# Kernel optimization log

Hardware: AMD Instinct MI355X
Metric: run time of the kernel (lower is better)

Reference implementation:

```python
import jax, jax.numpy as jnp
import numpy as np

SHAPES = ((496, 432), (248, 216), (124, 108))
NS = (40000, 20000, 8000)
T = 32
B = 4
EPS = 1e-3


def _bn(x, g, b, m, v):
    return (x - m) * (g / jnp.sqrt(v + EPS)) + b


def _vfe_scale(voxels, num_pts, w1, p1, w2, p2):
    # voxels: (N, T, 4); num_pts: (N,)
    Tp = voxels.shape[1]
    n = num_pts.astype(voxels.dtype)[:, None, None]
    m3 = voxels[:, :, :3].sum(axis=1, keepdims=True) / n
    m2 = voxels[:, :, :2].sum(axis=1, keepdims=True) / n
    feat = jnp.concatenate([voxels[:, :, :4], voxels[:, :, :3] - m3, voxels[:, :, :2] - m2], axis=-1)  # (N,T,9)
    mask = (jnp.arange(Tp)[None, :] < num_pts[:, None]).astype(voxels.dtype)[:, :, None]
    x = feat
    for w, (g, b_, rm, rv) in ((w1, p1), (w2, p2)):
        h = jax.nn.relu(_bn(jnp.einsum('ntc,cd->ntd', x, w), g, b_, rm, rv))  # (N,T,64)
        gmax = h.max(axis=1, keepdims=True)  # global max includes padded rows, as in torch source
        x = jnp.concatenate([h, jnp.broadcast_to(gmax, h.shape)], axis=-1) * mask  # (N,T,128)
    return x.max(axis=1)[:, :64]  # (N,64)


def _scatter_bev(vf, coords, h, w, batch_size):
    b = coords[:, 0]
    y = jnp.clip(coords[:, 2], 0, h - 1)
    x = jnp.clip(coords[:, 3], 0, w - 1)
    grid = jnp.zeros((batch_size, vf.shape[1], h, w), vf.dtype)
    return grid.at[b, :, y, x].set(vf)


def _fusion(x, w, g, b, m, v):
    y = jax.lax.conv_general_dilated(x, w, (1, 1), ((1, 1), (1, 1)),
                                     dimension_numbers=('NCHW', 'OIHW', 'NCHW'))
    y = _bn(y, g[None, :, None, None], b[None, :, None, None], m[None, :, None, None], v[None, :, None, None])
    return jax.nn.relu(y)


def setup_inputs() -> dict:
    key = jax.random.key(0)
    ks = jax.random.split(key, 32)
    inp = {}
    for s in range(3):
        h, w = SHAPES[s]
        inp[f'voxels_{s}'] = jax.random.normal(ks[s], (NS[s], T, 4), dtype=jnp.float32)
        inp[f'num_pts_{s}'] = jax.random.randint(ks[3 + s], (NS[s],), 1, T + 1, dtype=jnp.int32)
        b = jax.random.randint(ks[6 + s], (NS[s],), 0, B, dtype=jnp.int32)
        z = jnp.zeros((NS[s],), jnp.int32)
        y = jax.random.randint(ks[9 + s], (NS[s],), 0, h, dtype=jnp.int32)
        x = jax.random.randint(ks[12 + s], (NS[s],), 0, w, dtype=jnp.int32)
        inp[f'coords_{s}'] = jnp.stack([b, z, y, x], axis=1)
    # VFE params (stacked across the 3 scales; identical shapes per scale)
    inp['w1'] = jax.random.normal(ks[15], (3, 9, 64), dtype=jnp.float32) * 0.1
    inp['g1'] = jnp.ones((3, 64), jnp.float32) + 0.1 * jax.random.normal(ks[16], (3, 64))
    inp['b1'] = 0.05 * jax.random.normal(ks[17], (3, 64))
    inp['rm1'] = 0.05 * jax.random.normal(ks[18], (3, 64))
    inp['rv1'] = 0.5 + jnp.abs(jax.random.normal(ks[19], (3, 64)))
    inp['w2'] = jax.random.normal(ks[20], (3, 128, 64), dtype=jnp.float32) * 0.05
    inp['g2'] = jnp.ones((3, 64), jnp.float32) + 0.1 * jax.random.normal(ks[21], (3, 64))
    inp['b2'] = 0.05 * jax.random.normal(ks[22], (3, 64))
    inp['rm2'] = 0.05 * jax.random.normal(ks[23], (3, 64))
    inp['rv2'] = 0.5 + jnp.abs(jax.random.normal(ks[24], (3, 64)))
    # Fusion convs (2): Conv2d(128,64,3) + BN
    inp['fw'] = jax.random.normal(ks[25], (2, 64, 128, 3, 3), dtype=jnp.float32) * 0.03
    inp['fg'] = jnp.ones((2, 64), jnp.float32) + 0.1 * jax.random.normal(ks[26], (2, 64))
    inp['fb'] = 0.05 * jax.random.normal(ks[27], (2, 64))
    inp['fm'] = 0.05 * jax.random.normal(ks[28], (2, 64))
    inp['fv'] = 0.5 + jnp.abs(jax.random.normal(ks[29], (2, 64)))
    inp['batch_size'] = B
    return inp


def reference(voxels_0, voxels_1, voxels_2,
              w1, g1, b1, rm1, rv1, w2, g2, b2, rm2, rv2,
              fw, fg, fb, fm, fv,
              num_pts_0, num_pts_1, num_pts_2,
              coords_0, coords_1, coords_2, batch_size):
    voxels = (voxels_0, voxels_1, voxels_2)
    num_pts = (num_pts_0, num_pts_1, num_pts_2)
    coords = (coords_0, coords_1, coords_2)
    sf = []
    for s in range(3):
        vf = _vfe_scale(voxels[s], num_pts[s],
                        w1[s], (g1[s], b1[s], rm1[s], rv1[s]),
                        w2[s], (g2[s], b2[s], rm2[s], rv2[s]))
        h, w = SHAPES[s]
        sf.append(_scatter_bev(vf, coords[s], h, w, batch_size))
    # bottom-up fusion: scale2 -> scale1 -> scale0
    up = jax.image.resize(sf[2], sf[1].shape[:2] + SHAPES[1], method='bilinear')
    fused_1 = _fusion(jnp.concatenate([sf[1], up], axis=1), fw[1], fg[1], fb[1], fm[1], fv[1])
    up = jax.image.resize(fused_1, fused_1.shape[:2] + SHAPES[0], method='bilinear')
    fused_0 = _fusion(jnp.concatenate([sf[0], up], axis=1), fw[0], fg[0], fb[0], fm[0], fv[0])
    return fused_0  # spatial_features_2d: (B, 64, 496, 432)
```

## Files before the change

### kernel.cpp

```cpp
#include <hip/hip_runtime.h>

typedef unsigned short u16;
typedef short bf16x8 __attribute__((ext_vector_type(8)));
typedef float f32x4 __attribute__((ext_vector_type(4)));

#define EPSV 1e-3f

__device__ __forceinline__ float bf2f(u16 u) {
  union { unsigned int i; float f; } x; x.i = ((unsigned int)u) << 16; return x.f;
}
__device__ __forceinline__ u16 f2bf(float f) {
  union { float f; unsigned int i; } x; x.f = f;
  unsigned int r = x.i + 0x7fffu + ((x.i >> 16) & 1u);
  return (u16)(r >> 16);
}

#define WAVE_FENCE() do { __builtin_amdgcn_s_waitcnt(0); __builtin_amdgcn_wave_barrier(); } while (0)

__global__ void twt_kernel(const float* __restrict__ fw, u16* __restrict__ fwT) {
  int i = blockIdx.x * blockDim.x + threadIdx.x;
  if (i >= 2 * 9 * 64 * 128) return;
  int ci = i & 127;
  int r = i >> 7;
  int co = r & 63; r >>= 6;
  int kyx = r % 9;
  int set = r / 9;
  fwT[i] = f2bf(fw[(((set * 64 + co) * 128 + ci) * 9) + kyx]);
}

__global__ __launch_bounds__(256, 2) void vfe_mfma_kernel(
    const float* __restrict__ vox, const int* __restrict__ npts,
    const float* __restrict__ w1, const float* __restrict__ g1, const float* __restrict__ b1,
    const float* __restrict__ rm1, const float* __restrict__ rv1,
    const float* __restrict__ w2, const float* __restrict__ g2, const float* __restrict__ b2,
    const float* __restrict__ rm2, const float* __restrict__ rv2,
    float* __restrict__ vf, int N)
{
  struct PerWave {
    u16 X[32 * 72];
    u16 F[32 * 40];
    u16 G[64];
  };
  __shared__ __align__(16) union {
    struct { u16 W1T[64 * 40]; u16 W2T[64 * 136]; } w;
    PerWave r[4];
  } lds;

  const int tid = threadIdx.x;
  const int lane = tid & 63;
  const int wv = tid >> 6;
  const int m16 = lane & 15;
  const int q = lane >> 4;

  for (int i = tid; i < 64 * 40; i += 256) {
    int c = i / 40, k = i % 40;
    lds.w.W1T[i] = f2bf(k < 9 ? w1[k * 64 + c] : 0.f);
  }
  for (int i = tid; i < 64 * 136; i += 256) {
    int c = i / 136, j = i % 136;
    lds.w.W2T[i] = f2bf(j < 128 ? w2[j * 64 + c] : 0.f);
  }
  __syncthreads();

  bf16x8 bW1[4], bLo[4][2], bHi[4][2];
  float sc1[4], sh1[4], sc2[4], sh2[4];
#pragma unroll
  for (int nf = 0; nf < 4; ++nf) {
    int c = nf * 16 + m16;
    bW1[nf] = *(const bf16x8*)&lds.w.W1T[c * 40 + q * 8];
#pragma unroll
    for (int ks = 0; ks < 2; ++ks) {
      bLo[nf][ks] = *(const bf16x8*)&lds.w.W2T[c * 136 + ks * 32 + q * 8];
      bHi[nf][ks] = *(const bf16x8*)&lds.w.W2T[c * 136 + 64 + ks * 32 + q * 8];
    }
    float s1 = g1[c] * rsqrtf(rv1[c] + EPSV);
    sc1[nf] = s1; sh1[nf] = b1[c] - rm1[c] * s1;
    float s2 = g2[c] * rsqrtf(rv2[c] + EPSV);
    sc2[nf] = s2; sh2[nf] = b2[c] - rm2[c] * s2;
  }
  __syncthreads();

  u16* X = lds.r[wv].X;
  u16* F = lds.r[wv].F;
  u16* G = lds.r[wv].G;
  for (int i = lane; i < 640; i += 64) ((unsigned int*)F)[i] = 0u;

  const int wgid = blockIdx.x * 4 + wv;
  const int wstride = gridDim.x * 4;

  for (int v = wgid; v < N; v += wstride) {
    const int n = npts[v];
    float px = 0.f, py = 0.f, pz = 0.f, pw = 0.f;
    if (lane < 32) {
      float4 u = *(const float4*)(vox + ((size_t)v * 32 + lane) * 4);
      px = u.x; py = u.y; pz = u.z; pw = u.w;
    }
    float sx = px, sy = py, sz = pz;
#pragma unroll
    for (int off = 32; off >= 1; off >>= 1) {
      sx += __shfl_xor(sx, off);
      sy += __shfl_xor(sy, off);
      sz += __shfl_xor(sz, off);
    }
    float nf_ = (float)n;
    float mx = sx / nf_, my = sy / nf_, mz = sz / nf_;
    if (lane < 32) {
      float dx = px - mx, dy = py - my, dz = pz - mz;
      bf16x8 r0, r1;
      r0[0] = (short)f2bf(px); r0[1] = (short)f2bf(py);
      r0[2] = (short)f2bf(pz); r0[3] = (short)f2bf(pw);
      r0[4] = (short)f2bf(dx); r0[5] = (short)f2bf(dy);
      r0[6] = (short)f2bf(dz); r0[7] = (short)f2bf(dx);
      r1 = (bf16x8){0, 0, 0, 0, 0, 0, 0, 0};
      r1[0] = (short)f2bf(dy);
      *(bf16x8*)&F[lane * 40 + 0] = r0;
      *(bf16x8*)&F[lane * 40 + 8] = r1;
    }
    WAVE_FENCE();

    bf16x8 a1[2];
    a1[0] = *(const bf16x8*)&F[m16 * 40 + q * 8];
    a1[1] = *(const bf16x8*)&F[(16 + m16) * 40 + q * 8];
    f32x4 acc1[2][4];
#pragma unroll
    for (int mf = 0; mf < 2; ++mf)
#pragma unroll
      for (int nf = 0; nf < 4; ++nf) {
        acc1[mf][nf] = (f32x4){0.f, 0.f, 0.f, 0.f};
        acc1[mf][nf] = __builtin_amdgcn_mfma_f32_16x16x32_bf16(a1[mf], bW1[nf], acc1[mf][nf], 0, 0, 0);
      }

    float gmx[4] = {0.f, 0.f, 0.f, 0.f};
#pragma unroll
    for (int mf = 0; mf < 2; ++mf)
#pragma unroll
      for (int nf = 0; nf < 4; ++nf)
#pragma unroll
        for (int r = 0; r < 4; ++r) {
          float h = fmaxf(acc1[mf][nf][r] * sc1[nf] + sh1[nf], 0.f);
          gmx[nf] = fmaxf(gmx[nf], h);
          int t = mf * 16 + q * 4 + r;
          X[t * 72 + nf * 16 + m16] = f2bf(h);
        }
#pragma unroll
    for (int nf = 0; nf < 4; ++nf) {
      gmx[nf] = fmaxf(gmx[nf], __shfl_xor(gmx[nf], 16));
      gmx[nf] = fmaxf(gmx[nf], __shfl_xor(gmx[nf], 32));
    }
    if (q == 0) {
#pragma unroll
      for (int nf = 0; nf < 4; ++nf) G[nf * 16 + m16] = f2bf(gmx[nf]);
    }
    WAVE_FENCE();

    f32x4 ga[4];
#pragma unroll
    for (int nf = 0; nf < 4; ++nf) ga[nf] = (f32x4){0.f, 0.f, 0.f, 0.f};
#pragma unroll
    for (int ks = 0; ks < 2; ++ks) {
      bf16x8 ag = (bf16x8){0, 0, 0, 0, 0, 0, 0, 0};
      if (m16 == 0) ag = *(const bf16x8*)&G[ks * 32 + q * 8];
#pragma unroll
      for (int nf = 0; nf < 4; ++nf)
        ga[nf] = __builtin_amdgcn_mfma_f32_16x16x32_bf16(ag, bHi[nf][ks], ga[nf], 0, 0, 0);
    }
    float gt[4];
#pragma unroll
    for (int nf = 0; nf < 4; ++nf) {
      float s = ga[nf][0] + ga[nf][1] + ga[nf][2] + ga[nf][3];
      s += __shfl_xor(s, 16);
      s += __shfl_xor(s, 32);
      gt[nf] = s;
    }

    f32x4 acc2[2][4];
#pragma unroll
    for (int mf = 0; mf < 2; ++mf)
#pragma unroll
      for (int nf = 0; nf < 4; ++nf)
        acc2[mf][nf] = (f32x4){gt[nf], gt[nf], gt[nf], gt[nf]};
#pragma unroll
    for (int ks = 0; ks < 2; ++ks) {
      bf16x8 a2[2];
      a2[0] = *(const bf16x8*)&X[m16 * 72 + ks * 32 + q * 8];
      a2[1] = *(const bf16x8*)&X[(16 + m16) * 72 + ks * 32 + q * 8];
#pragma unroll
      for (int mf = 0; mf < 2; ++mf)
#pragma unroll
        for (int nf = 0; nf < 4; ++nf)
          acc2[mf][nf] = __builtin_amdgcn_mfma_f32_16x16x32_bf16(a2[mf], bLo[nf][ks], acc2[mf][nf], 0, 0, 0);
    }

    float vm[4] = {0.f, 0.f, 0.f, 0.f};
#pragma unroll
    for (int mf = 0; mf < 2; ++mf)
#pragma unroll
      for (int nf = 0; nf < 4; ++nf)
#pragma unroll
        for (int r = 0; r < 4; ++r) {
          int t = mf * 16 + q * 4 + r;
          float h2 = fmaxf(acc2[mf][nf][r] * sc2[nf] + sh2[nf], 0.f);
          if (t < n) vm[nf] = fmaxf(vm[nf], h2);
        }
#pragma unroll
    for (int nf = 0; nf < 4; ++nf) {
      vm[nf] = fmaxf(vm[nf], __shfl_xor(vm[nf], 16));
      vm[nf] = fmaxf(vm[nf], __shfl_xor(vm[nf], 32));
    }
    float outv = (q == 0) ? vm[0] : (q == 1) ? vm[1] : (q == 2) ? vm[2] : vm[3];
    vf[(size_t)v * 64 + q * 16 + m16] = outv;
    __builtin_amdgcn_wave_barrier();
  }
}

__global__ void winner_kernel(const int* __restrict__ coords, int* __restrict__ win,
                              int N, int H, int W) {
  int v = blockIdx.x * blockDim.x + threadIdx.x;
  if (v >= N) return;
  int b = coords[v * 4 + 0];
  int y = min(max(coords[v * 4 + 2], 0), H - 1);
  int x = min(max(coords[v * 4 + 3], 0), W - 1);
  atomicMax(&win[(b * H + y) * W + x], v);
}

__global__ void fill_kernel(const int* __restrict__ win, const float* __restrict__ vf,
                            u16* __restrict__ dst, int cells, int cstride) {
  int i = blockIdx.x * blockDim.x + threadIdx.x;
  if (i >= cells * 8) return;
  int cell = i >> 3, c8 = (i & 7) * 8;
  int wv = win[cell];
  bf16x8 o = (bf16x8){0, 0, 0, 0, 0, 0, 0, 0};
  if (wv >= 0) {
    const float* p = vf + (size_t)wv * 64 + c8;
    float4 v0 = *(const float4*)p;
    float4 v1 = *(const float4*)(p + 4);
    o[0] = (short)f2bf(v0.x); o[1] = (short)f2bf(v0.y);
    o[2] = (short)f2bf(v0.z); o[3] = (short)f2bf(v0.w);
    o[4] = (short)f2bf(v1.x); o[5] = (short)f2bf(v1.y);
    o[6] = (short)f2bf(v1.z); o[7] = (short)f2bf(v1.w);
  }
  *(bf16x8*)&dst[(size_t)cell * cstride + c8] = o;
}

__global__ void upsample_kernel(const u16* __restrict__ src, u16* __restrict__ dst,
                                int Hc, int Wc, int dstride, int doff, int total8) {
  int i = blockIdx.x * blockDim.x + threadIdx.x;
  if (i >= total8) return;
  int c8 = (i & 7) * 8;
  int px = i >> 3;
  int W2 = Wc * 2, H2 = Hc * 2;
  int x = px % W2; int t = px / W2; int y = t % H2; int n = t / H2;
  int ky = y >> 1, kx = x >> 1;
  int ya, yb, xa, xb; float wya, wxa;
  if ((y & 1) == 0) { ya = ky > 0 ? ky - 1 : 0; yb = ky; wya = 0.25f; }
  else              { ya = ky; yb = (ky + 1 < Hc) ? ky + 1 : Hc - 1; wya = 0.75f; }
  if ((x & 1) == 0) { xa = kx > 0 ? kx - 1 : 0; xb = kx; wxa = 0.25f; }
  else              { xa = kx; xb = (kx + 1 < Wc) ? kx + 1 : Wc - 1; wxa = 0.75f; }
  float wyb = 1.f - wya, wxb = 1.f - wxa;
  const u16* sp = src + c8;
  bf16x8 vaa = *(const bf16x8*)&sp[((size_t)(n * Hc + ya) * Wc + xa) * 64];
  bf16x8 vab = *(const bf16x8*)&sp[((size_t)(n * Hc + ya) * Wc + xb) * 64];
  bf16x8 vba = *(const bf16x8*)&sp[((size_t)(n * Hc + yb) * Wc + xa) * 64];
  bf16x8 vbb = *(const bf16x8*)&sp[((size_t)(n * Hc + yb) * Wc + xb) * 64];
  bf16x8 o;
#pragma unroll
  for (int j = 0; j < 8; ++j) {
    float v = wya * (wxa * bf2f((u16)vaa[j]) + wxb * bf2f((u16)vab[j])) +
              wyb * (wxa * bf2f((u16)vba[j]) + wxb * bf2f((u16)vbb[j]));
    o[j] = (short)f2bf(v);
  }
  *(bf16x8*)&dst[(size_t)px * dstride + doff + c8] = o;
}

template<int H, int W, bool NCHW_OUT>
__global__ __launch_bounds__(256, 2) void conv_kernel(
    const u16* __restrict__ in, const u16* __restrict__ wT,
    const float* __restrict__ fg, const float* __restrict__ fb,
    const float* __restrict__ fm, const float* __restrict__ fv,
    void* __restrict__ outv)
{
  constexpr int XT = 32, YT = 8;
  constexpr int XTILES = (W + XT - 1) / XT;
  constexpr int CIP = 72;
  constexpr int NPX = 10 * 34;
  __shared__ __align__(16) union {
    struct { u16 A[NPX * CIP]; u16 B[2][64 * CIP]; } s;
    float T[4 * 64 * 33];
  } lds;

  const int tid = threadIdx.x;
  const int lane = tid & 63;
  const int wv = tid >> 6;
  const int m16 = lane & 15;
  const int q = lane >> 4;

  int bid = blockIdx.x;
  const int xt = bid % XTILES; bid /= XTILES;
  const int yt = bid % (H / YT);
  const int n = bid / (H / YT);
  const int x0 = xt * XT, y0 = yt * YT;

  float sc[4], sh[4];
#pragma unroll
  for (int nf = 0; nf < 4; ++nf) {
    int co = nf * 16 + m16;
    float s = fg[co] * rsqrtf(fv[co] + EPSV);
    sc[nf] = s;
    sh[nf] = fb[co] - fm[co] * s;
  }

  f32x4 acc[4][4];
#pragma unroll
  for (int mf = 0; mf < 4; ++mf)
#pragma unroll
    for (int nf = 0; nf < 4; ++nf)
      acc[mf][nf] = (f32x4){0.f, 0.f, 0.f, 0.f};

  for (int hf = 0; hf < 2; ++hf) {
    {
      const int cis = (tid & 7) * 8;
#pragma unroll
      for (int it = 0; it < 11; ++it) {
        int p = (tid >> 3) + it * 32;
        if (p < NPX) {
          int r = p / 34, xx = p - r * 34;
          int gy = y0 - 1 + r, gx = x0 - 1 + xx;
          uint4 v = make_uint4(0, 0, 0, 0);
          if (gy >= 0 && gy < H && gx >= 0 && gx < W)
            v = *(const uint4*)(in + ((size_t)((n * H + gy) * W + gx) * 128 + hf * 64 + cis));
          *(uint4*)&lds.s.A[p * CIP + cis] = v;
        }
      }
    }
    {
#pragma unroll
      for (int it = 0; it < 2; ++it) {
        int e8 = (it * 256 + tid) * 8;
        int co = e8 >> 6, ci = e8 & 63;
        uint4 v = *(const uint4*)(wT + (co * 128 + hf * 64 + ci));
        *(uint4*)&lds.s.B[0][co * CIP + ci] = v;
      }
    }
    __syncthreads();

    for (int kyx = 0; kyx < 9; ++kyx) {
      if (kyx < 8) {
#pragma unroll
        for (int it = 0; it < 2; ++it) {
          int e8 = (it * 256 + tid) * 8;
          int co = e8 >> 6, ci = e8 & 63;
          uint4 v = *(const uint4*)(wT + ((kyx + 1) * 8192 + co * 128 + hf * 64 + ci));
          *(uint4*)&lds.s.B[(kyx + 1) & 1][co * CIP + ci] = v;
        }
      }
      const int ky = kyx / 3, kx = kyx - ky * 3;
      const u16* Bb = lds.s.B[kyx & 1];
#pragma unroll
      for (int cc = 0; cc < 2; ++cc) {
        bf16x8 a[4], b[4];
#pragma unroll
        for (int mf = 0; mf < 4; ++mf) {
          int p = (wv * 2 + (mf >> 1) + ky) * 34 + (mf & 1) * 16 + m16 + kx;
          a[mf] = *(const bf16x8*)&lds.s.A[p * CIP + cc * 32 + q * 8];
        }
#pragma unroll
        for (int nf = 0; nf < 4; ++nf)
          b[nf] = *(const bf16x8*)&Bb[(nf * 16 + m16) * CIP + cc * 32 + q * 8];
#pragma unroll
        for (int mf = 0; mf < 4; ++mf)
#pragma unroll
          for (int nf = 0; nf < 4; ++nf)
            acc[mf][nf] = __builtin_amdgcn_mfma_f32_16x16x32_bf16(a[mf], b[nf], acc[mf][nf], 0, 0, 0);
      }
      __syncthreads();
    }
  }

  if (!NCHW_OUT) {
    u16* out = (u16*)outv;
#pragma unroll
    for (int mf = 0; mf < 4; ++mf) {
      int y = y0 + wv * 2 + (mf >> 1);
#pragma unroll
      for (int nf = 0; nf < 4; ++nf)
#pragma unroll
        for (int r = 0; r < 4; ++r) {
          int px = (mf & 1) * 16 + q * 4 + r;
          int x = x0 + px;
          if (x < W) {
            int co = nf * 16 + m16;
            float v = fmaxf(acc[mf][nf][r] * sc[nf] + sh[nf], 0.f);
            out[((size_t)(n * H + y) * W + x) * 64 + co] = f2bf(v);
          }
        }
    }
  } else {
    float* out = (float*)outv;
    float* T = &lds.T[wv * 64 * 33];
#pragma unroll
    for (int yr = 0; yr < 2; ++yr) {
#pragma unroll
      for (int xc = 0; xc < 2; ++xc)
#pragma unroll
        for (int nf = 0; nf < 4; ++nf)
#pragma unroll
          for (int r = 0; r < 4; ++r) {
            int px = xc * 16 + q * 4 + r;
            int co = nf * 16 + m16;
            T[co * 33 + px] = fmaxf(acc[yr * 2 + xc][nf][r] * sc[nf] + sh[nf], 0.f);
          }
      WAVE_FENCE();
      const int px = lane & 31, co2 = lane >> 5;
      const int y = y0 + wv * 2 + yr;
      int x = x0 + px;
#pragma unroll 4
      for (int it = 0; it < 32; ++it) {
        int co = it * 2 + co2;
        float v = T[co * 33 + px];
        if (x < W) out[((size_t)(n * 64 + co) * H + y) * W + x] = v;
      }
      WAVE_FENCE();
    }
  }
}

extern "C" void kernel_launch(void* const* d_in, const int* in_sizes, int n_in,
                              void* d_out, int out_size, void* d_ws, size_t ws_size,
                              hipStream_t stream) {
  int I_vox[3], I_np[3], I_co[3];
  int I_w1, I_g1, I_b1, I_rm1, I_rv1, I_w2, I_g2, I_b2, I_rm2, I_rv2;
  int I_fw, I_fg, I_fb, I_fm, I_fv;
  if (in_sizes[1] == 40000) {
    I_vox[0] = 0; I_np[0] = 1; I_co[0] = 2;
    I_vox[1] = 3; I_np[1] = 4; I_co[1] = 5;
    I_vox[2] = 6; I_np[2] = 7; I_co[2] = 8;
    I_w1 = 9; I_g1 = 10; I_b1 = 11; I_rm1 = 12; I_rv1 = 13;
    I_w2 = 14; I_g2 = 15; I_b2 = 16; I_rm2 = 17; I_rv2 = 18;
    I_fw = 19; I_fg = 20; I_fb = 21; I_fm = 22; I_fv = 23;
  } else {
    I_vox[0] = 0; I_vox[1] = 1; I_vox[2] = 2;
    I_w1 = 3; I_g1 = 4; I_b1 = 5; I_rm1 = 6; I_rv1 = 7;
    I_w2 = 8; I_g2 = 9; I_b2 = 10; I_rm2 = 11; I_rv2 = 12;
    I_fw = 13; I_fg = 14; I_fb = 15; I_fm = 16; I_fv = 17;
    I_np[0] = 18; I_np[1] = 19; I_np[2] = 20;
    I_co[0] = 21; I_co[1] = 22; I_co[2] = 23;
  }

  const int HS[3] = {496, 248, 124};
  const int WS[3] = {432, 216, 108};
  int Nv[3];
  for (int s = 0; s < 3; ++s) Nv[s] = in_sizes[I_np[s]];

  char* wsp = (char*)d_ws;
  size_t off = 0;
  auto take = [&](size_t bytes) -> void* {
    void* p = wsp + off;
    off = (off + bytes + 255) & ~(size_t)255;
    return p;
  };
  float* vf[3]; int* win[3];
  for (int s = 0; s < 3; ++s) vf[s] = (float*)take((size_t)Nv[s] * 64 * 4);
  int cells[3];
  for (int s = 0; s < 3; ++s) {
    cells[s] = 4 * HS[s] * WS[s];
    win[s] = (int*)take((size_t)cells[s] * 4);
  }
  u16* buf0 = (u16*)take((size_t)cells[0] * 128 * 2);
  u16* buf1 = (u16*)take((size_t)cells[1] * 128 * 2);
  u16* g2b  = (u16*)take((size_t)cells[2] * 64 * 2);
  u16* fus1 = (u16*)take((size_t)cells[1] * 64 * 2);
  u16* fwT  = (u16*)take((size_t)2 * 9 * 64 * 128 * 2);

  const float* W1 = (const float*)d_in[I_w1];
  const float* G1 = (const float*)d_in[I_g1];
  const float* B1 = (const float*)d_in[I_b1];
  const float* RM1 = (const float*)d_in[I_rm1];
  const float* RV1 = (const float*)d_in[I_rv1];
  const float* W2 = (const float*)d_in[I_w2];
  const float* G2 = (const float*)d_in[I_g2];
  const float* B2 = (const float*)d_in[I_b2];
  const float* RM2 = (const float*)d_in[I_rm2];
  const float* RV2 = (const float*)d_in[I_rv2];
  const float* FW = (const float*)d_in[I_fw];
  const float* FG = (const float*)d_in[I_fg];
  const float* FB = (const float*)d_in[I_fb];
  const float* FM = (const float*)d_in[I_fm];
  const float* FV = (const float*)d_in[I_fv];

  for (int s = 0; s < 3; ++s)
    hipMemsetAsync(win[s], 0xFF, (size_t)cells[s] * 4, stream);

  twt_kernel<<<(2 * 9 * 64 * 128 + 255) / 256, 256, 0, stream>>>(FW, fwT);

  for (int s = 0; s < 3; ++s) {
    int blocks = (Nv[s] + 3) / 4;
    if (blocks > 1024) blocks = 1024;
    vfe_mfma_kernel<<<blocks, 256, 0, stream>>>(
        (const float*)d_in[I_vox[s]], (const int*)d_in[I_np[s]],
        W1 + s * 9 * 64, G1 + s * 64, B1 + s * 64, RM1 + s * 64, RV1 + s * 64,
        W2 + s * 128 * 64, G2 + s * 64, B2 + s * 64, RM2 + s * 64, RV2 + s * 64,
        vf[s], Nv[s]);
  }
  for (int s = 0; s < 3; ++s) {
    winner_kernel<<<(Nv[s] + 255) / 256, 256, 0, stream>>>(
        (const int*)d_in[I_co[s]], win[s], Nv[s], HS[s], WS[s]);
  }
  fill_kernel<<<(cells[0] * 8 + 255) / 256, 256, 0, stream>>>(win[0], vf[0], buf0, cells[0], 128);
  fill_kernel<<<(cells[1] * 8 + 255) / 256, 256, 0, stream>>>(win[1], vf[1], buf1, cells[1], 128);
  fill_kernel<<<(cells[2] * 8 + 255) / 256, 256, 0, stream>>>(win[2], vf[2], g2b, cells[2], 64);

  {
    int total8 = cells[1] * 8;
    upsample_kernel<<<(total8 + 255) / 256, 256, 0, stream>>>(g2b, buf1, 124, 108, 128, 64, total8);
  }
  conv_kernel<248, 216, false><<<4 * (248 / 8) * 7, 256, 0, stream>>>(
      buf1, fwT + 9 * 64 * 128, FG + 64, FB + 64, FM + 64, FV + 64, fus1);
  {
    int total8 = cells[0] * 8;
    upsample_kernel<<<(total8 + 255) / 256, 256, 0, stream>>>(fus1, buf0, 248, 216, 128, 64, total8);
  }
  conv_kernel<496, 432, true><<<4 * (496 / 8) * 14, 256, 0, stream>>>(
      buf0, fwT, FG, FB, FM, FV, (float*)d_out);
}
```

Before: 769.9 us.

## Load conv weights directly from global into registers, drop LDS weight staging

The 3x3 conv kernel no longer stages weights through a double-buffered LDS array. Each lane now loads its B fragments straight from global memory (likely L2-cached) per kernel tap, which removes the per-tap __syncthreads and shrinks LDS so launch bounds can request 3 blocks per CU. BN scale/shift computation is moved after the main loop to cut register pressure. The trade-off is more global or cache traffic for weights and higher per-lane register use for b fragments, which could conflict with the tighter occupancy target.

```diff
diff --git a/kernel.cpp b/kernel.cpp
--- a/kernel.cpp
+++ b/kernel.cpp
@@ -273,7 +273,7 @@
 }
 
 template<int H, int W, bool NCHW_OUT>
-__global__ __launch_bounds__(256, 2) void conv_kernel(
+__global__ __launch_bounds__(256, 3) void conv_kernel(
     const u16* __restrict__ in, const u16* __restrict__ wT,
     const float* __restrict__ fg, const float* __restrict__ fb,
     const float* __restrict__ fm, const float* __restrict__ fv,
@@ -284,7 +284,7 @@
   constexpr int CIP = 72;
   constexpr int NPX = 10 * 34;
   __shared__ __align__(16) union {
-    struct { u16 A[NPX * CIP]; u16 B[2][64 * CIP]; } s;
+    u16 A[NPX * CIP];
     float T[4 * 64 * 33];
   } lds;
 
@@ -300,14 +300,7 @@
   const int n = bid / (H / YT);
   const int x0 = xt * XT, y0 = yt * YT;
 
-  float sc[4], sh[4];
-#pragma unroll
-  for (int nf = 0; nf < 4; ++nf) {
-    int co = nf * 16 + m16;
-    float s = fg[co] * rsqrtf(fv[co] + EPSV);
-    sc[nf] = s;
-    sh[nf] = fb[co] - fm[co] * s;
-  }
+  const int boff = m16 * 128 + q * 8;
 
   f32x4 acc[4][4];
 #pragma unroll
@@ -317,6 +310,7 @@
       acc[mf][nf] = (f32x4){0.f, 0.f, 0.f, 0.f};
 
   for (int hf = 0; hf < 2; ++hf) {
+    if (hf) __syncthreads();
     {
       const int cis = (tid & 7) * 8;
 #pragma unroll
@@ -328,52 +322,46 @@
           uint4 v = make_uint4(0, 0, 0, 0);
           if (gy >= 0 && gy < H && gx >= 0 && gx < W)
             v = *(const uint4*)(in + ((size_t)((n * H + gy) * W + gx) * 128 + hf * 64 + cis));
-          *(uint4*)&lds.s.A[p * CIP + cis] = v;
+          *(uint4*)&lds.A[p * CIP + cis] = v;
         }
       }
     }
-    {
-#pragma unroll
-      for (int it = 0; it < 2; ++it) {
-        int e8 = (it * 256 + tid) * 8;
-        int co = e8 >> 6, ci = e8 & 63;
-        uint4 v = *(const uint4*)(wT + (co * 128 + hf * 64 + ci));
-        *(uint4*)&lds.s.B[0][co * CIP + ci] = v;
+    __syncthreads();
+
+#pragma unroll
+    for (int kyx = 0; kyx < 9; ++kyx) {
+      const int ky = kyx / 3, kx = kyx - ky * 3;
+      const u16* wp = wT + kyx * 8192 + hf * 64 + boff;
+      bf16x8 b[2][4];
+#pragma unroll
+      for (int nf = 0; nf < 4; ++nf) {
+        b[0][nf] = *(const bf16x8*)(wp + nf * 2048);
+        b[1][nf] = *(const bf16x8*)(wp + nf * 2048 + 32);
       }
-    }
-    __syncthreads();
-
-    for (int kyx = 0; kyx < 9; ++kyx) {
-      if (kyx < 8) {
-#pragma unroll
-        for (int it = 0; it < 2; ++it) {
-          int e8 = (it * 256 + tid) * 8;
-          int co = e8 >> 6, ci = e8 & 63;
-          uint4 v = *(const uint4*)(wT + ((kyx + 1) * 8192 + co * 128 + hf * 64 + ci));
-          *(uint4*)&lds.s.B[(kyx + 1) & 1][co * CIP + ci] = v;
-        }
-      }
-      const int ky = kyx / 3, kx = kyx - ky * 3;
-      const u16* Bb = lds.s.B[kyx & 1];
 #pragma unroll
       for (int cc = 0; cc < 2; ++cc) {
-        bf16x8 a[4], b[4];
+        bf16x8 a[4];
 #pragma unroll
         for (int mf = 0; mf < 4; ++mf) {
           int p = (wv * 2 + (mf >> 1) + ky) * 34 + (mf & 1) * 16 + m16 + kx;
-          a[mf] = *(const bf16x8*)&lds.s.A[p * CIP + cc * 32 + q * 8];
+          a[mf] = *(const bf16x8*)&lds.A[p * CIP + cc * 32 + q * 8];
         }
 #pragma unroll
-        for (int nf = 0; nf < 4; ++nf)
-          b[nf] = *(const bf16x8*)&Bb[(nf * 16 + m16) * CIP + cc * 32 + q * 8];
-#pragma unroll
         for (int mf = 0; mf < 4; ++mf)
 #pragma unroll
           for (int nf = 0; nf < 4; ++nf)
-            acc[mf][nf] = __builtin_amdgcn_mfma_f32_16x16x32_bf16(a[mf], b[nf], acc[mf][nf], 0, 0, 0);
+            acc[mf][nf] = __builtin_amdgcn_mfma_f32_16x16x32_bf16(a[mf], b[cc][nf], acc[mf][nf], 0, 0, 0);
       }
-      __syncthreads();
-    }
+    }
+  }
+
+  float sc[4], sh[4];
+#pragma unroll
+  for (int nf = 0; nf < 4; ++nf) {
+    int co = nf * 16 + m16;
+    float s = fg[co] * rsqrtf(fv[co] + EPSV);
+    sc[nf] = s;
+    sh[nf] = fb[co] - fm[co] * s;
   }
 
   if (!NCHW_OUT) {
@@ -395,6 +383,7 @@
         }
     }
   } else {
+    __syncthreads();
     float* out = (float*)outv;
     float* T = &lds.T[wv * 64 * 33];
 #pragma unroll
```

Result: slower. 1.028 ms (+33.5%).
